# Optimization experiments

Measured on AMD Instinct MI355X. Metric: run time of the kernel, lower is better.

The kernel has to match this reference:

```python
import jax, jax.numpy as jnp
import numpy as np

N = 100000       # nodes
E = 1600000      # edges
F_IN = 128       # num_node_features
H = 256          # graph_hidden_channels
NHID = 512
NOUT = 256
G = 256          # graphs in batch


def setup_inputs() -> dict:
    key = jax.random.key(0)
    ks = jax.random.split(key, 14)
    x = jax.random.normal(ks[0], (N, F_IN), jnp.float32)
    src = jax.random.randint(ks[1], (E,), 0, N, jnp.int32)
    dst = jax.random.randint(ks[2], (E,), 0, N, jnp.int32)
    batch = jnp.sort(jax.random.randint(ks[3], (N,), 0, G, jnp.int32))
    def lin(k, fan_in, fan_out):
        return jax.random.normal(k, (fan_in, fan_out), jnp.float32) * (1.0 / np.sqrt(fan_in))
    return {
        "x": x, "src": src, "dst": dst, "batch": batch,
        "W1": lin(ks[4], F_IN, H), "b1": jnp.zeros((H,), jnp.float32),
        "W2": lin(ks[5], H, H),    "b2": jnp.zeros((H,), jnp.float32),
        "W3": lin(ks[6], H, H),    "b3": jnp.zeros((H,), jnp.float32),
        "Wm1": lin(ks[7], H, NHID), "bm1": jnp.zeros((NHID,), jnp.float32),
        "Wm2": lin(ks[8], NHID, NOUT), "bm2": jnp.zeros((NOUT,), jnp.float32),
    }


def _gcn_layer(h_in, W, b, src, dst, dinv):
    # GCNConv: transform, then symmetric-normalized aggregation with self-loops.
    h = h_in @ W                                            # [N, out]
    norm = (dinv[src] * dinv[dst])[:, None]                 # [E, 1]
    agg = jax.ops.segment_sum(h[src] * norm, dst, num_segments=N)
    agg = agg + h * (dinv * dinv)[:, None]                  # self-loop term (norm = 1/deg)
    return agg + b


def reference(x, src, dst, batch, W1, b1, W2, b2, W3, b3, Wm1, bm1, Wm2, bm2):
    # degrees include the added self-loop (+1)
    deg = 1.0 + jax.ops.segment_sum(jnp.ones((E,), x.dtype), dst, num_segments=N)
    dinv = jax.lax.rsqrt(deg)                               # deg^{-1/2}

    h = jax.nn.relu(_gcn_layer(x, W1, b1, src, dst, dinv))
    h = jax.nn.relu(_gcn_layer(h, W2, b2, src, dst, dinv))
    h = _gcn_layer(h, W3, b3, src, dst, dinv)               # no relu before pooling

    # global mean pool over graphs
    counts = jax.ops.segment_sum(jnp.ones((N,), x.dtype), batch, num_segments=G)
    pooled = jax.ops.segment_sum(h, batch, num_segments=G) / jnp.maximum(counts, 1.0)[:, None]

    out = jax.nn.relu(pooled @ Wm1 + bm1) @ Wm2 + bm2       # [G, NOUT]
    return out
```

## Files before the change

kernel.cpp:

```cpp
#include <hip/hip_runtime.h>
#include <hip/hip_bf16.h>

#define N_NODES 100000
#define N_EDGES 1600000
#define F_IN    128
#define H       256
#define NHID    512
#define NOUT    256
#define G_GR    256

typedef unsigned short u16;
typedef __attribute__((ext_vector_type(8))) short s16x8;
typedef __attribute__((ext_vector_type(8))) unsigned short u16x8;
typedef __attribute__((ext_vector_type(4))) float f32x4;

__device__ __forceinline__ float bf2f(u16 u) {
    union { unsigned int i; float f; } v; v.i = ((unsigned int)u) << 16; return v.f;
}
__device__ __forceinline__ u16 f2bf(float f) {
    union { float f; unsigned int i; } v; v.f = f;
    unsigned int x = v.i;
    x += 0x7fffu + ((x >> 16) & 1u);
    return (u16)(x >> 16);
}

#define CD_BLKS   1563
#define SPX_BLKS  ((N_NODES * F_IN) / 1024)
#define T1_BLKS   ((F_IN * H) / 256)
#define T2_BLKS   ((H * H) / 256)
#define HEAD_BLKS (CD_BLKS + SPX_BLKS + T1_BLKS + T2_BLKS + 2)

__device__ __forceinline__ void transpose_split_body(const float* __restrict__ W,
        u16* __restrict__ thi, u16* __restrict__ tlo, int K, int N, int id) {
    int n = id / K, k = id - n * K;
    float f = W[(size_t)k * N + n];
    u16 h = f2bf(f);
    thi[id] = h;
    tlo[id] = f2bf(f - bf2f(h));
}

__global__ __launch_bounds__(256) void prep_head(
        const int* __restrict__ dst, int* __restrict__ degc,
        const float* __restrict__ x, u16* __restrict__ x_bf,
        const float* __restrict__ W1, u16* __restrict__ t1h, u16* __restrict__ t1l,
        const float* __restrict__ W2, u16* __restrict__ t2h, u16* __restrict__ t2l,
        const int* __restrict__ batch, int* __restrict__ goff) {
    int bid = blockIdx.x;
    if (bid < CD_BLKS) {
        int base = bid * 1024 + threadIdx.x;
#pragma unroll
        for (int q = 0; q < 4; q++) {
            int e = base + q * 256;
            if (e < N_EDGES) atomicAdd(&degc[dst[e]], 1);
        }
        return;
    }
    bid -= CD_BLKS;
    if (bid < SPX_BLKS) {
        int idx = bid * 256 + threadIdx.x;
        float4 f = *(const float4*)&x[(size_t)idx * 4];
        ushort4 o;
        o.x = f2bf(f.x); o.y = f2bf(f.y); o.z = f2bf(f.z); o.w = f2bf(f.w);
        *(ushort4*)&x_bf[(size_t)idx * 4] = o;
        return;
    }
    bid -= SPX_BLKS;
    if (bid < T1_BLKS) {
        transpose_split_body(W1, t1h, t1l, F_IN, H, bid * 256 + threadIdx.x);
        return;
    }
    bid -= T1_BLKS;
    if (bid < T2_BLKS) {
        transpose_split_body(W2, t2h, t2l, H, H, bid * 256 + threadIdx.x);
        return;
    }
    bid -= T2_BLKS;
    {
        int g = bid * 256 + threadIdx.x;
        if (g > G_GR) return;
        int lo = 0, hi = N_NODES;
        while (lo < hi) {
            int mid = (lo + hi) >> 1;
            if (batch[mid] < g) lo = mid + 1; else hi = mid;
        }
        goff[g] = lo;
    }
}

__global__ void scan_partial(const int* __restrict__ cnt, int* __restrict__ partial) {
    __shared__ int s[256];
    int t = threadIdx.x;
    int i = blockIdx.x * 256 + t;
    int v = (i < N_NODES) ? cnt[i] : 0;
    s[t] = v; __syncthreads();
    for (int off = 128; off > 0; off >>= 1) {
        if (t < off) s[t] += s[t + off];
        __syncthreads();
    }
    if (t == 0) partial[blockIdx.x] = s[0];
}

__global__ void scan_offsets(int* __restrict__ partial, int nb, int* __restrict__ rowp) {
    __shared__ int s[512];
    int t = threadIdx.x;
    int orig = (t < nb) ? partial[t] : 0;
    s[t] = orig; __syncthreads();
    for (int off = 1; off < 512; off <<= 1) {
        int u = (t >= off) ? s[t - off] : 0;
        __syncthreads();
        s[t] += u;
        __syncthreads();
    }
    if (t < nb) partial[t] = s[t] - orig;
    if (t == 0) rowp[N_NODES] = N_EDGES;
}

__global__ void scan_final_dinv(const int* __restrict__ cnt, const int* __restrict__ partial,
                                int* __restrict__ rowp, int* __restrict__ cur,
                                float* __restrict__ dinv) {
    __shared__ int s[256];
    int t = threadIdx.x;
    int i = blockIdx.x * 256 + t;
    int v = (i < N_NODES) ? cnt[i] : 0;
    s[t] = v; __syncthreads();
    for (int off = 1; off < 256; off <<= 1) {
        int u = (t >= off) ? s[t - off] : 0;
        __syncthreads();
        s[t] += u;
        __syncthreads();
    }
    if (i < N_NODES) {
        int r = partial[blockIdx.x] + s[t] - v;
        rowp[i] = r;
        cur[i] = r;
        dinv[i] = rsqrtf(1.0f + (float)v);
    }
}

__global__ __launch_bounds__(256) void scatter_edges(
        const int* __restrict__ src, const int* __restrict__ dst,
        const float* __restrict__ dinv, int* __restrict__ cur,
        int2* __restrict__ ep) {
    int base = blockIdx.x * 1024 + threadIdx.x;
#pragma unroll
    for (int q = 0; q < 4; q++) {
        int e = base + q * 256;
        if (e < N_EDGES) {
            int d = dst[e];
            int s = src[e];
            float w = dinv[d] * dinv[s];
            int pos = atomicAdd(&cur[d], 1);
            int2 v; v.x = s; v.y = __float_as_int(w);
            ep[pos] = v;
        }
    }
}

__global__ __launch_bounds__(256) void gcn_agg256(
        const u16* __restrict__ in, const int* __restrict__ rowp,
        const int2* __restrict__ ep, const float* __restrict__ dinv,
        u16* __restrict__ outp) {
    int node = blockIdx.x * 8 + (threadIdx.x >> 5);
    int l = threadIdx.x & 31;
    int beg = rowp[node], end = rowp[node + 1];
    float a[8] = {};
    int e = beg;
    int2 pr[8];
    bool have = (e + 8 <= end);
    if (have) {
#pragma unroll
        for (int q = 0; q < 8; q++) pr[q] = ep[e + q];
    }
    while (have) {
        int2 g8[8];
#pragma unroll
        for (int q = 0; q < 8; q++) g8[q] = pr[q];
        int en = e + 8;
        bool haven = (en + 8 <= end);
        if (haven) {
#pragma unroll
            for (int q = 0; q < 8; q++) pr[q] = ep[en + q];
        }
#pragma unroll
        for (int q = 0; q < 8; q++) {
            u16x8 u = *(const u16x8*)&in[(size_t)g8[q].x * H + l * 8];
            float wt = __int_as_float(g8[q].y);
#pragma unroll
            for (int r = 0; r < 8; r++) a[r] += bf2f(u[r]) * wt;
        }
        e = en; have = haven;
    }
    for (; e < end; e++) {
        int2 pe = ep[e];
        float wt = __int_as_float(pe.y);
        u16x8 u = *(const u16x8*)&in[(size_t)pe.x * H + l * 8];
#pragma unroll
        for (int r = 0; r < 8; r++) a[r] += bf2f(u[r]) * wt;
    }
    float di = dinv[node];
    u16x8 us = *(const u16x8*)&in[(size_t)node * H + l * 8];
    float dd = di * di;
    u16x8 o;
#pragma unroll
    for (int r = 0; r < 8; r++) o[r] = f2bf(a[r] + bf2f(us[r]) * dd);
    *(u16x8*)&outp[(size_t)node * H + l * 8] = o;
}

__global__ __launch_bounds__(256) void gcn_agg128(
        const u16* __restrict__ in, const int* __restrict__ rowp,
        const int2* __restrict__ ep, const float* __restrict__ dinv,
        u16* __restrict__ outp) {
    int node = blockIdx.x * 16 + (threadIdx.x >> 4);
    int l = threadIdx.x & 15;
    int beg = rowp[node], end = rowp[node + 1];
    float a[8] = {};
    int e = beg;
    int2 pr[8];
    bool have = (e + 8 <= end);
    if (have) {
#pragma unroll
        for (int q = 0; q < 8; q++) pr[q] = ep[e + q];
    }
    while (have) {
        int2 g8[8];
#pragma unroll
        for (int q = 0; q < 8; q++) g8[q] = pr[q];
        int en = e + 8;
        bool haven = (en + 8 <= end);
        if (haven) {
#pragma unroll
            for (int q = 0; q < 8; q++) pr[q] = ep[en + q];
        }
#pragma unroll
        for (int q = 0; q < 8; q++) {
            u16x8 u = *(const u16x8*)&in[(size_t)g8[q].x * F_IN + l * 8];
            float wt = __int_as_float(g8[q].y);
#pragma unroll
            for (int r = 0; r < 8; r++) a[r] += bf2f(u[r]) * wt;
        }
        e = en; have = haven;
    }
    for (; e < end; e++) {
        int2 pe = ep[e];
        float wt = __int_as_float(pe.y);
        u16x8 u = *(const u16x8*)&in[(size_t)pe.x * F_IN + l * 8];
#pragma unroll
        for (int r = 0; r < 8; r++) a[r] += bf2f(u[r]) * wt;
    }
    float di = dinv[node];
    u16x8 us = *(const u16x8*)&in[(size_t)node * F_IN + l * 8];
    float dd = di * di;
    u16x8 o;
#pragma unroll
    for (int r = 0; r < 8; r++) o[r] = f2bf(a[r] + bf2f(us[r]) * dd);
    *(u16x8*)&outp[(size_t)node * F_IN + l * 8] = o;
}

template<int K, bool RELU>
__global__ __launch_bounds__(256) void gemm_bias(
        const u16* __restrict__ A,
        const u16* __restrict__ Bhi, const u16* __restrict__ Blo,
        const float* __restrict__ bias, u16* __restrict__ C, int M) {
    __shared__ __align__(16) u16 sA[128 * 40];
    __shared__ __align__(16) u16 sB[2 * 128 * 40];
    const int tid = threadIdx.x;
    const int w = tid >> 6, l = tid & 63;
    const int wm = (w & 1) * 64, wn = (w >> 1) * 64;
    const int bm = blockIdx.x * 128, bn = blockIdx.y * 128;
    const int srow = tid >> 2;
    const int schunk = (tid & 3) * 8;
    const int lr = l & 15, lg = (l >> 4) * 8;

    f32x4 acc[4][4] = {};

    for (int k0 = 0; k0 < K; k0 += 32) {
        {
            int r0 = bm + srow, r1 = bm + srow + 64;
            u16x8 v0 = {}, v1 = {};
            if (r0 < M) v0 = *(const u16x8*)&A[(size_t)r0 * K + k0 + schunk];
            if (r1 < M) v1 = *(const u16x8*)&A[(size_t)r1 * K + k0 + schunk];
            *(u16x8*)&sA[srow * 40 + schunk] = v0;
            *(u16x8*)&sA[(srow + 64) * 40 + schunk] = v1;
        }
        {
            int n0 = bn + srow, n1 = bn + srow + 64;
            *(u16x8*)&sB[srow * 40 + schunk] = *(const u16x8*)&Bhi[(size_t)n0 * K + k0 + schunk];
            *(u16x8*)&sB[(srow + 64) * 40 + schunk] = *(const u16x8*)&Bhi[(size_t)n1 * K + k0 + schunk];
            *(u16x8*)&sB[128 * 40 + srow * 40 + schunk] = *(const u16x8*)&Blo[(size_t)n0 * K + k0 + schunk];
            *(u16x8*)&sB[128 * 40 + (srow + 64) * 40 + schunk] = *(const u16x8*)&Blo[(size_t)n1 * K + k0 + schunk];
        }
        __syncthreads();

        s16x8 af[4], bh[4], bl[4];
#pragma unroll
        for (int i = 0; i < 4; i++)
            af[i] = __builtin_bit_cast(s16x8, *(const u16x8*)&sA[(wm + i * 16 + lr) * 40 + lg]);
#pragma unroll
        for (int j = 0; j < 4; j++) {
            bh[j] = __builtin_bit_cast(s16x8, *(const u16x8*)&sB[(wn + j * 16 + lr) * 40 + lg]);
            bl[j] = __builtin_bit_cast(s16x8, *(const u16x8*)&sB[128 * 40 + (wn + j * 16 + lr) * 40 + lg]);
        }
#pragma unroll
        for (int i = 0; i < 4; i++) {
#pragma unroll
            for (int j = 0; j < 4; j++) {
                acc[i][j] = __builtin_amdgcn_mfma_f32_16x16x32_bf16(af[i], bh[j], acc[i][j], 0, 0, 0);
                acc[i][j] = __builtin_amdgcn_mfma_f32_16x16x32_bf16(af[i], bl[j], acc[i][j], 0, 0, 0);
            }
        }
        __syncthreads();
    }

    float bcol[4];
#pragma unroll
    for (int j = 0; j < 4; j++) bcol[j] = bias[bn + wn + j * 16 + lr];

    const int lq = (l >> 4) * 4;
#pragma unroll
    for (int i = 0; i < 4; i++) {
#pragma unroll
        for (int r0 = 0; r0 < 4; r0++) {
            int row = bm + wm + i * 16 + lq + r0;
            if (row < M) {
#pragma unroll
                for (int j = 0; j < 4; j++) {
                    float v = acc[i][j][r0] + bcol[j];
                    if (RELU) v = fmaxf(v, 0.f);
                    C[(size_t)row * H + bn + wn + j * 16 + lr] = f2bf(v);
                }
            }
        }
    }
}

__global__ __launch_bounds__(256) void pool_mlp(
        const u16* __restrict__ a3, const int* __restrict__ goff,
        const float* __restrict__ W3, const float* __restrict__ b3,
        const float* __restrict__ Wm1, const float* __restrict__ bm1,
        const float* __restrict__ Wm2, const float* __restrict__ bm2,
        float* __restrict__ out) {
    __shared__ float p[H];
    __shared__ float y[H];
    __shared__ float hid[NHID];
    int g = blockIdx.x, t = threadIdx.x;
    int beg = goff[g], end = goff[g + 1];
    float acc = 0.f;
    for (int i = beg; i < end; i++) acc += bf2f(a3[(size_t)i * H + t]);
    p[t] = acc / fmaxf((float)(end - beg), 1.f);
    __syncthreads();
    {
        float a = b3[t];
        for (int k = 0; k < H; k++) a += p[k] * W3[(size_t)k * H + t];
        y[t] = a;
    }
    __syncthreads();
#pragma unroll
    for (int rep = 0; rep < 2; rep++) {
        int o = rep * 256 + t;
        float a = bm1[o];
        for (int k = 0; k < H; k++) a += y[k] * Wm1[(size_t)k * NHID + o];
        hid[o] = fmaxf(a, 0.f);
    }
    __syncthreads();
    float a = bm2[t];
    for (int k = 0; k < NHID; k++) a += hid[k] * Wm2[(size_t)k * NOUT + t];
    out[g * NOUT + t] = a;
}

extern "C" void kernel_launch(void* const* d_in, const int* in_sizes, int n_in,
                              void* d_out, int out_size, void* d_ws, size_t ws_size,
                              hipStream_t stream) {
    const float* x   = (const float*)d_in[0];
    const int*   src = (const int*)d_in[1];
    const int*   dst = (const int*)d_in[2];
    const int*   bat = (const int*)d_in[3];
    const float* W1  = (const float*)d_in[4];  const float* b1  = (const float*)d_in[5];
    const float* W2  = (const float*)d_in[6];  const float* b2  = (const float*)d_in[7];
    const float* W3  = (const float*)d_in[8];  const float* b3  = (const float*)d_in[9];
    const float* Wm1 = (const float*)d_in[10]; const float* bm1 = (const float*)d_in[11];
    const float* Wm2 = (const float*)d_in[12]; const float* bm2 = (const float*)d_in[13];
    float* out = (float*)d_out;

    char* p = (char*)d_ws;
    auto carve = [&](size_t bytes) -> void* {
        void* r = (void*)p;
        p += (bytes + 511) & ~(size_t)511;
        return r;
    };
    u16*   x_bf    = (u16*)  carve((size_t)N_NODES * F_IN * 2);
    u16*   aggX    = (u16*)  carve((size_t)N_NODES * F_IN * 2);
    u16*   bufA    = (u16*)  carve((size_t)N_NODES * H * 2);
    u16*   bufB    = (u16*)  carve((size_t)N_NODES * H * 2);
    float* dinv    = (float*)carve((size_t)N_NODES * 4);
    int*   degc    = (int*)  carve((size_t)N_NODES * 4);
    int*   rowp    = (int*)  carve((size_t)(N_NODES + 1) * 4);
    int*   cur     = (int*)  carve((size_t)N_NODES * 4);
    int2*  ep      = (int2*) carve((size_t)N_EDGES * 8);
    int*   partial = (int*)  carve(4096);
    int*   goff    = (int*)  carve((size_t)(G_GR + 1) * 4);
    u16*   Wt1_hi  = (u16*)  carve((size_t)F_IN * H * 2);
    u16*   Wt1_lo  = (u16*)  carve((size_t)F_IN * H * 2);
    u16*   Wt2_hi  = (u16*)  carve((size_t)H * H * 2);
    u16*   Wt2_lo  = (u16*)  carve((size_t)H * H * 2);

    const int NB = (N_NODES + 255) / 256;

    hipMemsetAsync(degc, 0, (size_t)N_NODES * 4, stream);
    prep_head<<<HEAD_BLKS, 256, 0, stream>>>(dst, degc, x, x_bf,
                                             W1, Wt1_hi, Wt1_lo,
                                             W2, Wt2_hi, Wt2_lo, bat, goff);
    scan_partial<<<NB, 256, 0, stream>>>(degc, partial);
    scan_offsets<<<1, 512, 0, stream>>>(partial, NB, rowp);
    scan_final_dinv<<<NB, 256, 0, stream>>>(degc, partial, rowp, cur, dinv);
    scatter_edges<<<CD_BLKS, 256, 0, stream>>>(src, dst, dinv, cur, ep);

    dim3 ggrid((N_NODES + 127) / 128, 2);

    gcn_agg128<<<N_NODES / 16, 256, 0, stream>>>(x_bf, rowp, ep, dinv, aggX);
    gemm_bias<F_IN, true><<<ggrid, 256, 0, stream>>>(aggX, Wt1_hi, Wt1_lo, b1, bufA, N_NODES);
    gcn_agg256<<<N_NODES / 8, 256, 0, stream>>>(bufA, rowp, ep, dinv, bufB);
    gemm_bias<H, true><<<ggrid, 256, 0, stream>>>(bufB, Wt2_hi, Wt2_lo, b2, bufA, N_NODES);
    gcn_agg256<<<N_NODES / 8, 256, 0, stream>>>(bufA, rowp, ep, dinv, bufB);

    pool_mlp<<<G_GR, 256, 0, stream>>>(bufB, goff, W3, b3, Wm1, bm1, Wm2, bm2, out);
}
```

Before: 785.8 us.

## Replace per-graph scalar MLP tail with split-bf16 MFMA GEMMs after pooling

The fused pool+MLP kernel, where each of 256 blocks ran serial fp32 dot products over W3, Wm1 and Wm2, is split in two. A pooling kernel writes hi/lo bf16 pooled features, and three small MFMA GEMM launches use split-precision (hi*hi + hi*lo + lo*hi) weights that are transposed in the prep kernel. This removes the redundant per-graph reads of the weight matrices and the scalar FMA chains. In exchange it adds launches, extra prep blocks, and GEMMs that use only a few workgroups.

```diff
diff --git a/kernel.cpp b/kernel.cpp
--- a/kernel.cpp
+++ b/kernel.cpp
@@ -28,7 +28,10 @@
 #define SPX_BLKS  ((N_NODES * F_IN) / 1024)
 #define T1_BLKS   ((F_IN * H) / 256)
 #define T2_BLKS   ((H * H) / 256)
-#define HEAD_BLKS (CD_BLKS + SPX_BLKS + T1_BLKS + T2_BLKS + 2)
+#define T3_BLKS   ((H * H) / 256)
+#define TM1_BLKS  ((H * NHID) / 256)
+#define TM2_BLKS  ((NHID * NOUT) / 256)
+#define HEAD_BLKS (CD_BLKS + SPX_BLKS + T1_BLKS + T2_BLKS + T3_BLKS + TM1_BLKS + TM2_BLKS + 2)
 
 __device__ __forceinline__ void transpose_split_body(const float* __restrict__ W,
         u16* __restrict__ thi, u16* __restrict__ tlo, int K, int N, int id) {
@@ -44,6 +47,9 @@
         const float* __restrict__ x, u16* __restrict__ x_bf,
         const float* __restrict__ W1, u16* __restrict__ t1h, u16* __restrict__ t1l,
         const float* __restrict__ W2, u16* __restrict__ t2h, u16* __restrict__ t2l,
+        const float* __restrict__ W3, u16* __restrict__ t3h, u16* __restrict__ t3l,
+        const float* __restrict__ Wm1, u16* __restrict__ tm1h, u16* __restrict__ tm1l,
+        const float* __restrict__ Wm2, u16* __restrict__ tm2h, u16* __restrict__ tm2l,
         const int* __restrict__ batch, int* __restrict__ goff) {
     int bid = blockIdx.x;
     if (bid < CD_BLKS) {
@@ -75,6 +81,21 @@
         return;
     }
     bid -= T2_BLKS;
+    if (bid < T3_BLKS) {
+        transpose_split_body(W3, t3h, t3l, H, H, bid * 256 + threadIdx.x);
+        return;
+    }
+    bid -= T3_BLKS;
+    if (bid < TM1_BLKS) {
+        transpose_split_body(Wm1, tm1h, tm1l, H, NHID, bid * 256 + threadIdx.x);
+        return;
+    }
+    bid -= TM1_BLKS;
+    if (bid < TM2_BLKS) {
+        transpose_split_body(Wm2, tm2h, tm2l, NHID, NOUT, bid * 256 + threadIdx.x);
+        return;
+    }
+    bid -= TM2_BLKS;
     {
         int g = bid * 256 + threadIdx.x;
         if (g > G_GR) return;
@@ -333,38 +354,122 @@
     }
 }
 
-__global__ __launch_bounds__(256) void pool_mlp(
+template<int K, int NW, bool RELU, bool F32OUT>
+__global__ __launch_bounds__(256) void gemm_split(
+        const u16* __restrict__ Ahi, const u16* __restrict__ Alo,
+        const u16* __restrict__ Bhi, const u16* __restrict__ Blo,
+        const float* __restrict__ bias,
+        u16* __restrict__ Chi, u16* __restrict__ Clo, float* __restrict__ Cf,
+        int M) {
+    __shared__ __align__(16) u16 sA[2 * 128 * 40];
+    __shared__ __align__(16) u16 sB[2 * 128 * 40];
+    const int tid = threadIdx.x;
+    const int w = tid >> 6, l = tid & 63;
+    const int wm = (w & 1) * 64, wn = (w >> 1) * 64;
+    const int bm = blockIdx.x * 128, bn = blockIdx.y * 128;
+    const int srow = tid >> 2;
+    const int schunk = (tid & 3) * 8;
+    const int lr = l & 15, lg = (l >> 4) * 8;
+
+    f32x4 acc[4][4] = {};
+
+    for (int k0 = 0; k0 < K; k0 += 32) {
+        {
+            int r0 = bm + srow, r1 = bm + srow + 64;
+            u16x8 v0 = {}, v1 = {}, w0 = {}, w1 = {};
+            if (r0 < M) {
+                v0 = *(const u16x8*)&Ahi[(size_t)r0 * K + k0 + schunk];
+                w0 = *(const u16x8*)&Alo[(size_t)r0 * K + k0 + schunk];
+            }
+            if (r1 < M) {
+                v1 = *(const u16x8*)&Ahi[(size_t)r1 * K + k0 + schunk];
+                w1 = *(const u16x8*)&Alo[(size_t)r1 * K + k0 + schunk];
+            }
+            *(u16x8*)&sA[srow * 40 + schunk] = v0;
+            *(u16x8*)&sA[(srow + 64) * 40 + schunk] = v1;
+            *(u16x8*)&sA[128 * 40 + srow * 40 + schunk] = w0;
+            *(u16x8*)&sA[128 * 40 + (srow + 64) * 40 + schunk] = w1;
+        }
+        {
+            int n0 = bn + srow, n1 = bn + srow + 64;
+            *(u16x8*)&sB[srow * 40 + schunk] = *(const u16x8*)&Bhi[(size_t)n0 * K + k0 + schunk];
+            *(u16x8*)&sB[(srow + 64) * 40 + schunk] = *(const u16x8*)&Bhi[(size_t)n1 * K + k0 + schunk];
+            *(u16x8*)&sB[128 * 40 + srow * 40 + schunk] = *(const u16x8*)&Blo[(size_t)n0 * K + k0 + schunk];
+            *(u16x8*)&sB[128 * 40 + (srow + 64) * 40 + schunk] = *(const u16x8*)&Blo[(size_t)n1 * K + k0 + schunk];
+        }
+        __syncthreads();
+
+        s16x8 af[4], al[4], bh[4], bl[4];
+#pragma unroll
+        for (int i = 0; i < 4; i++) {
+            af[i] = __builtin_bit_cast(s16x8, *(const u16x8*)&sA[(wm + i * 16 + lr) * 40 + lg]);
+            al[i] = __builtin_bit_cast(s16x8, *(const u16x8*)&sA[128 * 40 + (wm + i * 16 + lr) * 40 + lg]);
+        }
+#pragma unroll
+        for (int j = 0; j < 4; j++) {
+            bh[j] = __builtin_bit_cast(s16x8, *(const u16x8*)&sB[(wn + j * 16 + lr) * 40 + lg]);
+            bl[j] = __builtin_bit_cast(s16x8, *(const u16x8*)&sB[128 * 40 + (wn + j * 16 + lr) * 40 + lg]);
+        }
+#pragma unroll
+        for (int i = 0; i < 4; i++) {
+#pragma unroll
+            for (int j = 0; j < 4; j++) {
+                acc[i][j] = __builtin_amdgcn_mfma_f32_16x16x32_bf16(af[i], bh[j], acc[i][j], 0, 0, 0);
+                acc[i][j] = __builtin_amdgcn_mfma_f32_16x16x32_bf16(af[i], bl[j], acc[i][j], 0, 0, 0);
+                acc[i][j] = __builtin_amdgcn_mfma_f32_16x16x32_bf16(al[i], bh[j], acc[i][j], 0, 0, 0);
+            }
+        }
+        __syncthreads();
+    }
+
+    float bcol[4];
+#pragma unroll
+    for (int j = 0; j < 4; j++) bcol[j] = bias[bn + wn + j * 16 + lr];
+
+    const int lq = (l >> 4) * 4;
+#pragma unroll
+    for (int i = 0; i < 4; i++) {
+#pragma unroll
+        for (int r0 = 0; r0 < 4; r0++) {
+            int row = bm + wm + i * 16 + lq + r0;
+            if (row < M) {
+#pragma unroll
+                for (int j = 0; j < 4; j++) {
+                    float v = acc[i][j][r0] + bcol[j];
+                    if (RELU) v = fmaxf(v, 0.f);
+                    size_t idx = (size_t)row * NW + bn + wn + j * 16 + lr;
+                    if (F32OUT) {
+                        Cf[idx] = v;
+                    } else {
+                        u16 hv = f2bf(v);
+                        Chi[idx] = hv;
+                        Clo[idx] = f2bf(v - bf2f(hv));
+                    }
+                }
+            }
+        }
+    }
+}
+
+__global__ __launch_bounds__(256) void pool_split(
         const u16* __restrict__ a3, const int* __restrict__ goff,
-        const float* __restrict__ W3, const float* __restrict__ b3,
-        const float* __restrict__ Wm1, const float* __restrict__ bm1,
-        const float* __restrict__ Wm2, const float* __restrict__ bm2,
-        float* __restrict__ out) {
-    __shared__ float p[H];
-    __shared__ float y[H];
-    __shared__ float hid[NHID];
+        u16* __restrict__ phi, u16* __restrict__ plo) {
     int g = blockIdx.x, t = threadIdx.x;
     int beg = goff[g], end = goff[g + 1];
     float acc = 0.f;
-    for (int i = beg; i < end; i++) acc += bf2f(a3[(size_t)i * H + t]);
-    p[t] = acc / fmaxf((float)(end - beg), 1.f);
-    __syncthreads();
-    {
-        float a = b3[t];
-        for (int k = 0; k < H; k++) a += p[k] * W3[(size_t)k * H + t];
-        y[t] = a;
-    }
-    __syncthreads();
-#pragma unroll
-    for (int rep = 0; rep < 2; rep++) {
-        int o = rep * 256 + t;
-        float a = bm1[o];
-        for (int k = 0; k < H; k++) a += y[k] * Wm1[(size_t)k * NHID + o];
-        hid[o] = fmaxf(a, 0.f);
-    }
-    __syncthreads();
-    float a = bm2[t];
-    for (int k = 0; k < NHID; k++) a += hid[k] * Wm2[(size_t)k * NOUT + t];
-    out[g * NOUT + t] = a;
+    int i = beg;
+    for (; i + 4 <= end; i += 4) {
+        float v0 = bf2f(a3[(size_t)(i + 0) * H + t]);
+        float v1 = bf2f(a3[(size_t)(i + 1) * H + t]);
+        float v2 = bf2f(a3[(size_t)(i + 2) * H + t]);
+        float v3 = bf2f(a3[(size_t)(i + 3) * H + t]);
+        acc += (v0 + v1) + (v2 + v3);
+    }
+    for (; i < end; i++) acc += bf2f(a3[(size_t)i * H + t]);
+    acc /= fmaxf((float)(end - beg), 1.f);
+    u16 hv = f2bf(acc);
+    phi[g * H + t] = hv;
+    plo[g * H + t] = f2bf(acc - bf2f(hv));
 }
 
 extern "C" void kernel_launch(void* const* d_in, const int* in_sizes, int n_in,
@@ -402,13 +507,28 @@
     u16*   Wt1_lo  = (u16*)  carve((size_t)F_IN * H * 2);
     u16*   Wt2_hi  = (u16*)  carve((size_t)H * H * 2);
     u16*   Wt2_lo  = (u16*)  carve((size_t)H * H * 2);
+    u16*   Wt3_hi  = (u16*)  carve((size_t)H * H * 2);
+    u16*   Wt3_lo  = (u16*)  carve((size_t)H * H * 2);
+    u16*   Wm1t_hi = (u16*)  carve((size_t)H * NHID * 2);
+    u16*   Wm1t_lo = (u16*)  carve((size_t)H * NHID * 2);
+    u16*   Wm2t_hi = (u16*)  carve((size_t)NHID * NOUT * 2);
+    u16*   Wm2t_lo = (u16*)  carve((size_t)NHID * NOUT * 2);
+    u16*   p_hi    = (u16*)  carve((size_t)G_GR * H * 2);
+    u16*   p_lo    = (u16*)  carve((size_t)G_GR * H * 2);
+    u16*   y_hi    = (u16*)  carve((size_t)G_GR * H * 2);
+    u16*   y_lo    = (u16*)  carve((size_t)G_GR * H * 2);
+    u16*   hd_hi   = (u16*)  carve((size_t)G_GR * NHID * 2);
+    u16*   hd_lo   = (u16*)  carve((size_t)G_GR * NHID * 2);
 
     const int NB = (N_NODES + 255) / 256;
 
     hipMemsetAsync(degc, 0, (size_t)N_NODES * 4, stream);
     prep_head<<<HEAD_BLKS, 256, 0, stream>>>(dst, degc, x, x_bf,
                                              W1, Wt1_hi, Wt1_lo,
-                                             W2, Wt2_hi, Wt2_lo, bat, goff);
+                                             W2, Wt2_hi, Wt2_lo,
+                                             W3, Wt3_hi, Wt3_lo,
+                                             Wm1, Wm1t_hi, Wm1t_lo,
+                                             Wm2, Wm2t_hi, Wm2t_lo, bat, goff);
     scan_partial<<<NB, 256, 0, stream>>>(degc, partial);
     scan_offsets<<<1, 512, 0, stream>>>(partial, NB, rowp);
     scan_final_dinv<<<NB, 256, 0, stream>>>(degc, partial, rowp, cur, dinv);
@@ -422,5 +542,12 @@
     gemm_bias<H, true><<<ggrid, 256, 0, stream>>>(bufB, Wt2_hi, Wt2_lo, b2, bufA, N_NODES);
     gcn_agg256<<<N_NODES / 8, 256, 0, stream>>>(bufA, rowp, ep, dinv, bufB);
 
-    pool_mlp<<<G_GR, 256, 0, stream>>>(bufB, goff, W3, b3, Wm1, bm1, Wm2, bm2, out);
-}
+    pool_split<<<G_GR, 256, 0, stream>>>(bufB, goff, p_hi, p_lo);
+    dim3 g3(2, 2), gm1(2, 4), gm2(2, 2);
+    gemm_split<H, H, false, false><<<g3, 256, 0, stream>>>(
+        p_hi, p_lo, Wt3_hi, Wt3_lo, b3, y_hi, y_lo, nullptr, G_GR);
+    gemm_split<H, NHID, true, false><<<gm1, 256, 0, stream>>>(
+        y_hi, y_lo, Wm1t_hi, Wm1t_lo, bm1, hd_hi, hd_lo, nullptr, G_GR);
+    gemm_split<NHID, NOUT, false, true><<<gm2, 256, 0, stream>>>(
+        hd_hi, hd_lo, Wm2t_hi, Wm2t_lo, bm2, nullptr, nullptr, out, G_GR);
+}
```

New measurement: 752.1 us. 4.3% less time.
